# Performance work log

Hardware: AMD Instinct MI355X
Metric: run time of the kernel (lower is better)

Reference implementation:

```python
import jax, jax.numpy as jnp
import numpy as np
from jax import lax

T, B, V, N = 128, 256, 256, 1024


def setup_inputs() -> dict:
    key = jax.random.key(0)
    k1, k2, k3, k4 = jax.random.split(key, 4)
    inputs = jax.random.uniform(k1, (T, B, V), dtype=jnp.float32)
    labels = jax.random.uniform(k2, (T * B, V), dtype=jnp.float32)
    weights = jax.random.normal(k3, (V + N, N), dtype=jnp.float32) * 0.1
    bias = jnp.zeros((N,), dtype=jnp.float32)
    output_weights = jax.random.normal(k4, (N, V), dtype=jnp.float32) * 0.1
    output_bias = jnp.zeros((V,), dtype=jnp.float32)
    return {
        "inputs": inputs,
        "labels": labels,
        "weights": weights,
        "bias": bias,
        "output_weights": output_weights,
        "output_bias": output_bias,
    }


def reference(inputs, labels, weights, bias, output_weights, output_bias):
    t, b, v = inputs.shape
    n = weights.shape[1]
    # split concat-matmul into x@Wx + h@Wh (same math as concat([x,h]) @ W)
    w_x = weights[:v]   # [V, N]
    w_h = weights[v:]   # [N, N]

    def step(h, x):
        h_new = jnp.tanh(x @ w_x + h @ w_h + bias)
        return h_new, h_new

    h0 = jnp.zeros((b, n), dtype=inputs.dtype)
    _, outputs = lax.scan(step, h0, inputs)          # [T, B, N]
    outputs = outputs.reshape(t * b, n)              # concat over time
    logits = outputs @ output_weights + output_bias  # [T*B, V]
    # softmax_cross_entropy_with_logits (soft labels), then mean
    log_p = jax.nn.log_softmax(logits, axis=-1)
    loss = jnp.mean(-jnp.sum(labels * log_p, axis=-1))
    return loss
```

## Files before the change

### kernel.cpp

```cpp
#include <hip/hip_runtime.h>
#include <math.h>

typedef __bf16 bf16;
typedef __attribute__((ext_vector_type(4))) __bf16 bf16x4;
typedef __attribute__((ext_vector_type(8))) __bf16 bf16x8;
typedef __attribute__((ext_vector_type(4))) float f32x4;

#define T_STEPS 128
#define B_SZ    256
#define V_SZ    256
#define N_SZ    1024
#define NROWS   (T_STEPS * B_SZ)
#define RSTR    68
#define LSTR    17
#define NGRP    16
#define NCB     16

__device__ __forceinline__ float fast_tanh(float x) {
    float e = __expf(2.0f * x);
    return 1.0f - 2.0f / (e + 1.0f);
}

__device__ __forceinline__ bf16x8 cvt_bf16x8(float4 a, float4 b) {
    bf16x8 r;
    r[0] = (bf16)a.x; r[1] = (bf16)a.y; r[2] = (bf16)a.z; r[3] = (bf16)a.w;
    r[4] = (bf16)b.x; r[5] = (bf16)b.y; r[6] = (bf16)b.z; r[7] = (bf16)b.w;
    return r;
}

__global__ __launch_bounds__(256) void k_prep(
    const float* __restrict__ weights,
    const float* __restrict__ out_w,
    bf16* __restrict__ Wxt,
    bf16* __restrict__ Wht,
    bf16* __restrict__ Wot)
{
    __shared__ float tile[32][33];
    int id = blockIdx.x;
    const float* src; bf16* dst; int R, C, tr, tc;
    if (id < 256) {
        src = weights; dst = Wxt; R = V_SZ; C = N_SZ;
        tr = (id & 7) * 32; tc = (id >> 3) * 32;
    } else if (id < 1280) {
        id -= 256;
        src = weights + (size_t)V_SZ * N_SZ; dst = Wht; R = N_SZ; C = N_SZ;
        tr = (id & 31) * 32; tc = (id >> 5) * 32;
    } else {
        id -= 1280;
        src = out_w; dst = Wot; R = N_SZ; C = V_SZ;
        tr = (id & 31) * 32; tc = (id >> 5) * 32;
    }
    int tx = threadIdx.x & 31;
    int ty = threadIdx.x >> 5;
#pragma unroll
    for (int i = 0; i < 32; i += 8)
        tile[ty + i][tx] = src[(size_t)(tr + ty + i) * C + tc + tx];
    __syncthreads();
#pragma unroll
    for (int i = 0; i < 32; i += 8)
        dst[(size_t)(tc + ty + i) * R + tr + tx] = (bf16)tile[tx][ty + i];
}

__global__ __launch_bounds__(512, 2) void k_rnn(
    const float* __restrict__ Xf,
    const bf16* __restrict__ Wxt,
    const bf16* __restrict__ Wht,
    const bf16* __restrict__ Wot,
    const float* __restrict__ bias,
    bf16* __restrict__ XH,
    unsigned int* __restrict__ Lgu,
    int* __restrict__ flg)
{
    __shared__ float red[8 * 16 * RSTR];
    __shared__ float lred[8 * 16 * LSTR];
    const int tid  = threadIdx.x;
    const int lane = tid & 63;
    const int w    = tid >> 6;
    const int quad = lane >> 4;
    const int l15  = lane & 15;
    const int g  = blockIdx.x >> 4;
    const int c  = blockIdx.x & 15;
    const int m0 = g * 16;
    const int n0 = c * 64;
    const int k0 = w * 128;
    const int v0 = w * 32;
    int* gflg  = flg + g * (NCB * T_STEPS);
    int* myflg = gflg + c * T_STEPS;
    int* pflg  = gflg + (2 * w + (lane & 1)) * T_STEPS;

    const bf16* Bp = Wht + (size_t)(n0 + l15) * N_SZ + k0 + quad * 8;
    bf16x8 b[4][4];
#pragma unroll
    for (int nt = 0; nt < 4; ++nt)
#pragma unroll
        for (int kc = 0; kc < 4; ++kc)
            b[nt][kc] = *(const bf16x8*)&Bp[(size_t)(nt * 16) * N_SZ + kc * 32];
    bf16x8 bx[4];
#pragma unroll
    for (int nt = 0; nt < 4; ++nt)
        bx[nt] = *(const bf16x8*)&Wxt[(size_t)(n0 + nt * 16 + l15) * V_SZ + v0 + quad * 8];
    bf16x8 bo[4];
#pragma unroll
    for (int kc = 0; kc < 4; ++kc)
        bo[kc] = *(const bf16x8*)&Wot[(size_t)(c * 16 + l15) * N_SZ + k0 + kc * 32 + quad * 8];

    const int orow = tid >> 5;
    const int ocol = (tid & 31) * 2;
    const float bias0 = bias[n0 + ocol];
    const float bias1 = bias[n0 + ocol + 1];
    const int lrow = w * 2 + (lane >> 3);
    const int lvp  = lane & 7;
    unsigned int* XHu = (unsigned int*)XH;
    const f32x4 zz = {0.f, 0.f, 0.f, 0.f};
    const size_t xin = (size_t)(m0 + l15) * V_SZ + v0 + quad * 8;

    {
        float4 f0 = *(const float4*)&Xf[xin];
        float4 f1 = *(const float4*)&Xf[xin + 4];
        bf16x8 ax = cvt_bf16x8(f0, f1);
        f32x4 acc[4] = {zz, zz, zz, zz};
#pragma unroll
        for (int nt = 0; nt < 4; ++nt)
            acc[nt] = __builtin_amdgcn_mfma_f32_16x16x32_bf16(ax, bx[nt], acc[nt], 0, 0, 0);
#pragma unroll
        for (int nt = 0; nt < 4; ++nt)
#pragma unroll
            for (int r = 0; r < 4; ++r)
                red[(w * 16 + quad * 4 + r) * RSTR + nt * 16 + l15] = acc[nt][r];
        __syncthreads();
        float s0 = bias0, s1 = bias1;
#pragma unroll
        for (int w2 = 0; w2 < 8; ++w2) {
            float2 v = *(const float2*)&red[(w2 * 16 + orow) * RSTR + ocol];
            s0 += v.x; s1 += v.y;
        }
        bf16 r0 = (bf16)fast_tanh(s0);
        bf16 r1 = (bf16)fast_tanh(s1);
        unsigned int outw = (unsigned int)__builtin_bit_cast(unsigned short, r0)
                          | ((unsigned int)__builtin_bit_cast(unsigned short, r1) << 16);
        size_t oidx = (((size_t)m0 + orow) * N_SZ + n0 + ocol) >> 1;
        __hip_atomic_store(&XHu[oidx], outw, __ATOMIC_RELAXED, __HIP_MEMORY_SCOPE_AGENT);
        asm volatile("s_waitcnt vmcnt(0)" ::: "memory");
        __syncthreads();
        if (tid == 0)
            __hip_atomic_store(&myflg[0], 1, __ATOMIC_RELAXED, __HIP_MEMORY_SCOPE_AGENT);
    }

    for (int t = 1; t < T_STEPS; ++t) {
        float4 f0 = *(const float4*)&Xf[(size_t)t * B_SZ * V_SZ + xin];
        float4 f1 = *(const float4*)&Xf[(size_t)t * B_SZ * V_SZ + xin + 4];
        bf16x8 ax = cvt_bf16x8(f0, f1);
        f32x4 acc[4] = {zz, zz, zz, zz};
#pragma unroll
        for (int nt = 0; nt < 4; ++nt)
            acc[nt] = __builtin_amdgcn_mfma_f32_16x16x32_bf16(ax, bx[nt], acc[nt], 0, 0, 0);

        if (lane < 2) {
            while (__hip_atomic_load(&pflg[t - 1], __ATOMIC_RELAXED,
                                     __HIP_MEMORY_SCOPE_AGENT) == 0)
                __builtin_amdgcn_s_sleep(1);
        }
        asm volatile("" ::: "memory");

        const bf16* Ap = XH + ((size_t)(t - 1) * B_SZ + m0 + l15) * N_SZ + k0 + quad * 8;
        bf16x8 a[4];
#pragma unroll
        for (int kc = 0; kc < 4; ++kc)
            a[kc] = *(const bf16x8*)&Ap[kc * 32];

#pragma unroll
        for (int kc = 0; kc < 4; ++kc)
#pragma unroll
            for (int nt = 0; nt < 4; ++nt)
                acc[nt] = __builtin_amdgcn_mfma_f32_16x16x32_bf16(a[kc], b[nt][kc],
                                                                  acc[nt], 0, 0, 0);
#pragma unroll
        for (int nt = 0; nt < 4; ++nt)
#pragma unroll
            for (int r = 0; r < 4; ++r)
                red[(w * 16 + quad * 4 + r) * RSTR + nt * 16 + l15] = acc[nt][r];
        __syncthreads();

        float s0 = bias0, s1 = bias1;
#pragma unroll
        for (int w2 = 0; w2 < 8; ++w2) {
            float2 v = *(const float2*)&red[(w2 * 16 + orow) * RSTR + ocol];
            s0 += v.x; s1 += v.y;
        }
        bf16 r0 = (bf16)fast_tanh(s0);
        bf16 r1 = (bf16)fast_tanh(s1);
        unsigned int outw = (unsigned int)__builtin_bit_cast(unsigned short, r0)
                          | ((unsigned int)__builtin_bit_cast(unsigned short, r1) << 16);
        size_t oidx = (((size_t)t * B_SZ + m0 + orow) * N_SZ + n0 + ocol) >> 1;
        __hip_atomic_store(&XHu[oidx], outw, __ATOMIC_RELAXED, __HIP_MEMORY_SCOPE_AGENT);

        asm volatile("s_waitcnt vmcnt(0)" ::: "memory");
        __syncthreads();
        if (tid == 0)
            __hip_atomic_store(&myflg[t], 1, __ATOMIC_RELAXED, __HIP_MEMORY_SCOPE_AGENT);

        f32x4 lacc = zz;
#pragma unroll
        for (int kc = 0; kc < 4; ++kc)
            lacc = __builtin_amdgcn_mfma_f32_16x16x32_bf16(a[kc], bo[kc], lacc, 0, 0, 0);
#pragma unroll
        for (int r = 0; r < 4; ++r)
            lred[(w * 16 + quad * 4 + r) * LSTR + l15] = lacc[r];
        __syncthreads();
        if (lane < 16) {
            float sa = 0.f, sb = 0.f;
#pragma unroll
            for (int w2 = 0; w2 < 8; ++w2) {
                sa += lred[(w2 * 16 + lrow) * LSTR + lvp * 2];
                sb += lred[(w2 * 16 + lrow) * LSTR + lvp * 2 + 1];
            }
            bf16 pa = (bf16)sa, pb = (bf16)sb;
            unsigned int pw = (unsigned int)__builtin_bit_cast(unsigned short, pa)
                            | ((unsigned int)__builtin_bit_cast(unsigned short, pb) << 16);
            Lgu[(((size_t)(t - 1) * 16 + c) * B_SZ + m0 + lrow) * 8 + lvp] = pw;
        }
    }

    if (lane < 2) {
        while (__hip_atomic_load(&pflg[T_STEPS - 1], __ATOMIC_RELAXED,
                                 __HIP_MEMORY_SCOPE_AGENT) == 0)
            __builtin_amdgcn_s_sleep(1);
    }
    asm volatile("" ::: "memory");
    {
        const bf16* Ap = XH + ((size_t)(T_STEPS - 1) * B_SZ + m0 + l15) * N_SZ + k0 + quad * 8;
        bf16x8 a[4];
#pragma unroll
        for (int kc = 0; kc < 4; ++kc)
            a[kc] = *(const bf16x8*)&Ap[kc * 32];
        f32x4 lacc = zz;
#pragma unroll
        for (int kc = 0; kc < 4; ++kc)
            lacc = __builtin_amdgcn_mfma_f32_16x16x32_bf16(a[kc], bo[kc], lacc, 0, 0, 0);
        __syncthreads();
#pragma unroll
        for (int r = 0; r < 4; ++r)
            lred[(w * 16 + quad * 4 + r) * LSTR + l15] = lacc[r];
        __syncthreads();
        if (lane < 16) {
            float sa = 0.f, sb = 0.f;
#pragma unroll
            for (int w2 = 0; w2 < 8; ++w2) {
                sa += lred[(w2 * 16 + lrow) * LSTR + lvp * 2];
                sb += lred[(w2 * 16 + lrow) * LSTR + lvp * 2 + 1];
            }
            bf16 pa = (bf16)sa, pb = (bf16)sb;
            unsigned int pw = (unsigned int)__builtin_bit_cast(unsigned short, pa)
                            | ((unsigned int)__builtin_bit_cast(unsigned short, pb) << 16);
            Lgu[(((size_t)(T_STEPS - 1) * 16 + c) * B_SZ + m0 + lrow) * 8 + lvp] = pw;
        }
    }
}

__global__ __launch_bounds__(256) void k_lred(
    const bf16* __restrict__ Lg,
    const float* __restrict__ labels,
    const float* __restrict__ ob,
    float* __restrict__ out)
{
    __shared__ float bt[4];
    const int tid  = threadIdx.x;
    const int lane = tid & 63;
    const int w    = tid >> 6;
    const int cs   = lane >> 2;
    const int vi   = (lane & 3) * 4;
    const float4 ob4 = *(const float4*)&ob[cs * 16 + vi];

    float wtot = 0.f;
    for (int i = 0; i < 32; ++i) {
        int row  = blockIdx.x * 128 + w * 32 + i;
        int p    = row >> 8;
        int brow = row & 255;
        bf16x4 lv = *(const bf16x4*)&Lg[(((size_t)p * 16 + cs) * B_SZ + brow) * 16 + vi];
        float l0 = (float)lv.x + ob4.x;
        float l1 = (float)lv.y + ob4.y;
        float l2 = (float)lv.z + ob4.z;
        float l3 = (float)lv.w + ob4.w;
        float mx = fmaxf(fmaxf(l0, l1), fmaxf(l2, l3));
#pragma unroll
        for (int sft = 1; sft < 64; sft <<= 1)
            mx = fmaxf(mx, __shfl_xor(mx, sft, 64));
        float sume = __expf(l0 - mx) + __expf(l1 - mx) + __expf(l2 - mx) + __expf(l3 - mx);
        const float4 lb = *(const float4*)&labels[(size_t)row * V_SZ + cs * 16 + vi];
        float labs = lb.x + lb.y + lb.z + lb.w;
        float labv = lb.x * l0 + lb.y * l1 + lb.z * l2 + lb.w * l3;
#pragma unroll
        for (int sft = 1; sft < 64; sft <<= 1) {
            sume += __shfl_xor(sume, sft, 64);
            labs += __shfl_xor(labs, sft, 64);
            labv += __shfl_xor(labv, sft, 64);
        }
        float lse = mx + __logf(sume);
        wtot += labs * lse - labv;
    }
    if (lane == 0) bt[w] = wtot;
    __syncthreads();
    if (tid == 0)
        atomicAdd(out, (bt[0] + bt[1] + bt[2] + bt[3]) * (1.0f / (float)NROWS));
}

extern "C" void kernel_launch(void* const* d_in, const int* in_sizes, int n_in,
                              void* d_out, int out_size, void* d_ws, size_t ws_size,
                              hipStream_t stream)
{
    const float* inputs  = (const float*)d_in[0];
    const float* labels  = (const float*)d_in[1];
    const float* weights = (const float*)d_in[2];
    const float* bias    = (const float*)d_in[3];
    const float* out_w   = (const float*)d_in[4];
    const float* out_b   = (const float*)d_in[5];
    float* out = (float*)d_out;

    char* ws = (char*)d_ws;
    bf16* XH  = (bf16*)ws;  ws += (size_t)NROWS * N_SZ * 2;
    bf16* Lg  = (bf16*)ws;  ws += (size_t)NROWS * V_SZ * 2;
    bf16* Wxt = (bf16*)ws;  ws += (size_t)N_SZ * V_SZ * 2;
    bf16* Wht = (bf16*)ws;  ws += (size_t)N_SZ * N_SZ * 2;
    bf16* Wot = (bf16*)ws;  ws += (size_t)V_SZ * N_SZ * 2;
    int*  flg = (int*)ws;   ws += (size_t)NGRP * NCB * T_STEPS * 4;

    hipMemsetAsync(out, 0, sizeof(float), stream);
    hipMemsetAsync(flg, 0, (size_t)NGRP * NCB * T_STEPS * 4, stream);

    k_prep<<<dim3(1536), 256, 0, stream>>>(weights, out_w, Wxt, Wht, Wot);

    k_rnn<<<dim3(NGRP * NCB), 512, 0, stream>>>(inputs, Wxt, Wht, Wot, bias, XH,
                                                (unsigned int*)Lg, flg);

    k_lred<<<dim3(NROWS / 128), 256, 0, stream>>>(Lg, labels, out_b, out);
}
```

Before: 519.4 us.

## Give each RNN wave full-K ownership of one tile and move output projection into loss kernel

The recurrent kernel now assigns each wave a full 16x16 output tile over the whole K=1024 dimension with Wht held in registers. This removes the LDS cross-wave reduction and the __syncthreads calls per timestep, and flags become per-wave monotonic counters that all 64 lanes poll. The output projection and logits buffer are removed from the recurrence and recomputed in a separate tiled GEMM-plus-softmax loss kernel that reads XH. The trade-off is more register pressure (32+8 bf16x8 fragments), larger per-wave global loads of h each step, and more flag polling traffic.

New measurement: 1.138 ms. 2.19x slower.

```diff
diff --git a/kernel.cpp b/kernel.cpp
--- a/kernel.cpp
+++ b/kernel.cpp
@@ -2,7 +2,6 @@
 #include <math.h>
 
 typedef __bf16 bf16;
-typedef __attribute__((ext_vector_type(4))) __bf16 bf16x4;
 typedef __attribute__((ext_vector_type(8))) __bf16 bf16x8;
 typedef __attribute__((ext_vector_type(4))) float f32x4;
 
@@ -11,10 +10,8 @@
 #define V_SZ    256
 #define N_SZ    1024
 #define NROWS   (T_STEPS * B_SZ)
-#define RSTR    68
-#define LSTR    17
 #define NGRP    16
-#define NCB     16
+#define NTILE   64
 
 __device__ __forceinline__ float fast_tanh(float x) {
     float e = __expf(2.0f * x);
@@ -61,244 +58,206 @@
         dst[(size_t)(tc + ty + i) * R + tr + tx] = (bf16)tile[tx][ty + i];
 }
 
-__global__ __launch_bounds__(512, 2) void k_rnn(
+__global__ __launch_bounds__(256, 1) void k_rnn(
     const float* __restrict__ Xf,
     const bf16* __restrict__ Wxt,
     const bf16* __restrict__ Wht,
-    const bf16* __restrict__ Wot,
     const float* __restrict__ bias,
     bf16* __restrict__ XH,
-    unsigned int* __restrict__ Lgu,
     int* __restrict__ flg)
 {
-    __shared__ float red[8 * 16 * RSTR];
-    __shared__ float lred[8 * 16 * LSTR];
     const int tid  = threadIdx.x;
     const int lane = tid & 63;
     const int w    = tid >> 6;
     const int quad = lane >> 4;
     const int l15  = lane & 15;
-    const int g  = blockIdx.x >> 4;
-    const int c  = blockIdx.x & 15;
-    const int m0 = g * 16;
-    const int n0 = c * 64;
-    const int k0 = w * 128;
-    const int v0 = w * 32;
-    int* gflg  = flg + g * (NCB * T_STEPS);
-    int* myflg = gflg + c * T_STEPS;
-    int* pflg  = gflg + (2 * w + (lane & 1)) * T_STEPS;
-
-    const bf16* Bp = Wht + (size_t)(n0 + l15) * N_SZ + k0 + quad * 8;
-    bf16x8 b[4][4];
-#pragma unroll
-    for (int nt = 0; nt < 4; ++nt)
-#pragma unroll
-        for (int kc = 0; kc < 4; ++kc)
-            b[nt][kc] = *(const bf16x8*)&Bp[(size_t)(nt * 16) * N_SZ + kc * 32];
-    bf16x8 bx[4];
-#pragma unroll
-    for (int nt = 0; nt < 4; ++nt)
-        bx[nt] = *(const bf16x8*)&Wxt[(size_t)(n0 + nt * 16 + l15) * V_SZ + v0 + quad * 8];
-    bf16x8 bo[4];
-#pragma unroll
-    for (int kc = 0; kc < 4; ++kc)
-        bo[kc] = *(const bf16x8*)&Wot[(size_t)(c * 16 + l15) * N_SZ + k0 + kc * 32 + quad * 8];
-
-    const int orow = tid >> 5;
-    const int ocol = (tid & 31) * 2;
-    const float bias0 = bias[n0 + ocol];
-    const float bias1 = bias[n0 + ocol + 1];
-    const int lrow = w * 2 + (lane >> 3);
-    const int lvp  = lane & 7;
-    unsigned int* XHu = (unsigned int*)XH;
+    const int g    = blockIdx.x >> 4;
+    const int nt   = (blockIdx.x & 15) * 4 + w;
+    const int m0   = g * 16;
+    const int n0   = nt * 16;
+    int* gflg = flg + g * NTILE;
+
+    bf16x8 b[32];
+#pragma unroll
+    for (int kc = 0; kc < 32; ++kc)
+        b[kc] = *(const bf16x8*)&Wht[(size_t)(n0 + l15) * N_SZ + kc * 32 + quad * 8];
+    bf16x8 bx[8];
+#pragma unroll
+    for (int kc = 0; kc < 8; ++kc)
+        bx[kc] = *(const bf16x8*)&Wxt[(size_t)(n0 + l15) * V_SZ + kc * 32 + quad * 8];
+    const float4 bias4 = *(const float4*)&bias[n0 + quad * 4];
+
+    const size_t xbase = (size_t)(m0 + l15) * V_SZ + quad * 8;
+    const size_t hoff  = (size_t)(m0 + l15) * N_SZ + n0 + quad * 4;
     const f32x4 zz = {0.f, 0.f, 0.f, 0.f};
-    const size_t xin = (size_t)(m0 + l15) * V_SZ + v0 + quad * 8;
 
     {
-        float4 f0 = *(const float4*)&Xf[xin];
-        float4 f1 = *(const float4*)&Xf[xin + 4];
-        bf16x8 ax = cvt_bf16x8(f0, f1);
-        f32x4 acc[4] = {zz, zz, zz, zz};
-#pragma unroll
-        for (int nt = 0; nt < 4; ++nt)
-            acc[nt] = __builtin_amdgcn_mfma_f32_16x16x32_bf16(ax, bx[nt], acc[nt], 0, 0, 0);
-#pragma unroll
-        for (int nt = 0; nt < 4; ++nt)
-#pragma unroll
-            for (int r = 0; r < 4; ++r)
-                red[(w * 16 + quad * 4 + r) * RSTR + nt * 16 + l15] = acc[nt][r];
-        __syncthreads();
-        float s0 = bias0, s1 = bias1;
-#pragma unroll
-        for (int w2 = 0; w2 < 8; ++w2) {
-            float2 v = *(const float2*)&red[(w2 * 16 + orow) * RSTR + ocol];
-            s0 += v.x; s1 += v.y;
-        }
-        bf16 r0 = (bf16)fast_tanh(s0);
-        bf16 r1 = (bf16)fast_tanh(s1);
-        unsigned int outw = (unsigned int)__builtin_bit_cast(unsigned short, r0)
-                          | ((unsigned int)__builtin_bit_cast(unsigned short, r1) << 16);
-        size_t oidx = (((size_t)m0 + orow) * N_SZ + n0 + ocol) >> 1;
-        __hip_atomic_store(&XHu[oidx], outw, __ATOMIC_RELAXED, __HIP_MEMORY_SCOPE_AGENT);
+        f32x4 acc0 = zz, acc1 = zz;
+#pragma unroll
+        for (int kc = 0; kc < 8; ++kc) {
+            float4 f0 = *(const float4*)&Xf[xbase + kc * 32];
+            float4 f1 = *(const float4*)&Xf[xbase + kc * 32 + 4];
+            bf16x8 ax = cvt_bf16x8(f0, f1);
+            if (kc & 1) acc1 = __builtin_amdgcn_mfma_f32_16x16x32_bf16(bx[kc], ax, acc1, 0, 0, 0);
+            else        acc0 = __builtin_amdgcn_mfma_f32_16x16x32_bf16(bx[kc], ax, acc0, 0, 0, 0);
+        }
+        float s0 = acc0[0] + acc1[0] + bias4.x;
+        float s1 = acc0[1] + acc1[1] + bias4.y;
+        float s2 = acc0[2] + acc1[2] + bias4.z;
+        float s3 = acc0[3] + acc1[3] + bias4.w;
+        bf16 h0 = (bf16)fast_tanh(s0), h1 = (bf16)fast_tanh(s1);
+        bf16 h2 = (bf16)fast_tanh(s2), h3 = (bf16)fast_tanh(s3);
+        unsigned int lo = (unsigned int)__builtin_bit_cast(unsigned short, h0)
+                        | ((unsigned int)__builtin_bit_cast(unsigned short, h1) << 16);
+        unsigned int hi = (unsigned int)__builtin_bit_cast(unsigned short, h2)
+                        | ((unsigned int)__builtin_bit_cast(unsigned short, h3) << 16);
+        unsigned long long pk = (unsigned long long)lo | ((unsigned long long)hi << 32);
+        __hip_atomic_store((unsigned long long*)(XH + hoff), pk,
+                           __ATOMIC_RELAXED, __HIP_MEMORY_SCOPE_AGENT);
         asm volatile("s_waitcnt vmcnt(0)" ::: "memory");
-        __syncthreads();
-        if (tid == 0)
-            __hip_atomic_store(&myflg[0], 1, __ATOMIC_RELAXED, __HIP_MEMORY_SCOPE_AGENT);
+        if (lane == 0)
+            __hip_atomic_store(&gflg[nt], 1, __ATOMIC_RELAXED, __HIP_MEMORY_SCOPE_AGENT);
     }
 
     for (int t = 1; t < T_STEPS; ++t) {
-        float4 f0 = *(const float4*)&Xf[(size_t)t * B_SZ * V_SZ + xin];
-        float4 f1 = *(const float4*)&Xf[(size_t)t * B_SZ * V_SZ + xin + 4];
-        bf16x8 ax = cvt_bf16x8(f0, f1);
-        f32x4 acc[4] = {zz, zz, zz, zz};
-#pragma unroll
-        for (int nt = 0; nt < 4; ++nt)
-            acc[nt] = __builtin_amdgcn_mfma_f32_16x16x32_bf16(ax, bx[nt], acc[nt], 0, 0, 0);
-
-        if (lane < 2) {
-            while (__hip_atomic_load(&pflg[t - 1], __ATOMIC_RELAXED,
-                                     __HIP_MEMORY_SCOPE_AGENT) == 0)
-                __builtin_amdgcn_s_sleep(1);
+        f32x4 acc0 = zz, acc1 = zz;
+        const float* xp = &Xf[(size_t)t * B_SZ * V_SZ + xbase];
+#pragma unroll
+        for (int kc = 0; kc < 8; ++kc) {
+            float4 f0 = *(const float4*)&xp[kc * 32];
+            float4 f1 = *(const float4*)&xp[kc * 32 + 4];
+            bf16x8 ax = cvt_bf16x8(f0, f1);
+            if (kc & 1) acc1 = __builtin_amdgcn_mfma_f32_16x16x32_bf16(bx[kc], ax, acc1, 0, 0, 0);
+            else        acc0 = __builtin_amdgcn_mfma_f32_16x16x32_bf16(bx[kc], ax, acc0, 0, 0, 0);
+        }
+        asm volatile("" : "+v"(acc0), "+v"(acc1) :: "memory");
+
+        while (true) {
+            int v = __hip_atomic_load(&gflg[lane], __ATOMIC_RELAXED,
+                                      __HIP_MEMORY_SCOPE_AGENT);
+            if (__all(v >= t)) break;
+            __builtin_amdgcn_s_sleep(1);
         }
         asm volatile("" ::: "memory");
 
-        const bf16* Ap = XH + ((size_t)(t - 1) * B_SZ + m0 + l15) * N_SZ + k0 + quad * 8;
-        bf16x8 a[4];
-#pragma unroll
-        for (int kc = 0; kc < 4; ++kc)
+        const bf16* Ap = XH + ((size_t)(t - 1) * B_SZ + m0 + l15) * N_SZ + quad * 8;
+        bf16x8 a[32];
+#pragma unroll
+        for (int kc = 0; kc < 32; ++kc)
             a[kc] = *(const bf16x8*)&Ap[kc * 32];
-
-#pragma unroll
-        for (int kc = 0; kc < 4; ++kc)
-#pragma unroll
-            for (int nt = 0; nt < 4; ++nt)
-                acc[nt] = __builtin_amdgcn_mfma_f32_16x16x32_bf16(a[kc], b[nt][kc],
-                                                                  acc[nt], 0, 0, 0);
-#pragma unroll
-        for (int nt = 0; nt < 4; ++nt)
-#pragma unroll
-            for (int r = 0; r < 4; ++r)
-                red[(w * 16 + quad * 4 + r) * RSTR + nt * 16 + l15] = acc[nt][r];
-        __syncthreads();
-
-        float s0 = bias0, s1 = bias1;
-#pragma unroll
-        for (int w2 = 0; w2 < 8; ++w2) {
-            float2 v = *(const float2*)&red[(w2 * 16 + orow) * RSTR + ocol];
-            s0 += v.x; s1 += v.y;
-        }
-        bf16 r0 = (bf16)fast_tanh(s0);
-        bf16 r1 = (bf16)fast_tanh(s1);
-        unsigned int outw = (unsigned int)__builtin_bit_cast(unsigned short, r0)
-                          | ((unsigned int)__builtin_bit_cast(unsigned short, r1) << 16);
-        size_t oidx = (((size_t)t * B_SZ + m0 + orow) * N_SZ + n0 + ocol) >> 1;
-        __hip_atomic_store(&XHu[oidx], outw, __ATOMIC_RELAXED, __HIP_MEMORY_SCOPE_AGENT);
-
+#pragma unroll
+        for (int kc = 0; kc < 32; ++kc) {
+            if (kc & 1) acc1 = __builtin_amdgcn_mfma_f32_16x16x32_bf16(b[kc], a[kc], acc1, 0, 0, 0);
+            else        acc0 = __builtin_amdgcn_mfma_f32_16x16x32_bf16(b[kc], a[kc], acc0, 0, 0, 0);
+        }
+
+        float s0 = acc0[0] + acc1[0] + bias4.x;
+        float s1 = acc0[1] + acc1[1] + bias4.y;
+        float s2 = acc0[2] + acc1[2] + bias4.z;
+        float s3 = acc0[3] + acc1[3] + bias4.w;
+        bf16 h0 = (bf16)fast_tanh(s0), h1 = (bf16)fast_tanh(s1);
+        bf16 h2 = (bf16)fast_tanh(s2), h3 = (bf16)fast_tanh(s3);
+        unsigned int lo = (unsigned int)__builtin_bit_cast(unsigned short, h0)
+                        | ((unsigned int)__builtin_bit_cast(unsigned short, h1) << 16);
+        unsigned int hi = (unsigned int)__builtin_bit_cast(unsigned short, h2)
+                        | ((unsigned int)__builtin_bit_cast(unsigned short, h3) << 16);
+        unsigned long long pk = (unsigned long long)lo | ((unsigned long long)hi << 32);
+        __hip_atomic_store((unsigned long long*)(XH + (size_t)t * B_SZ * N_SZ + hoff), pk,
+                           __ATOMIC_RELAXED, __HIP_MEMORY_SCOPE_AGENT);
         asm volatile("s_waitcnt vmcnt(0)" ::: "memory");
-        __syncthreads();
-        if (tid == 0)
-            __hip_atomic_store(&myflg[t], 1, __ATOMIC_RELAXED, __HIP_MEMORY_SCOPE_AGENT);
-
-        f32x4 lacc = zz;
-#pragma unroll
-        for (int kc = 0; kc < 4; ++kc)
-            lacc = __builtin_amdgcn_mfma_f32_16x16x32_bf16(a[kc], bo[kc], lacc, 0, 0, 0);
-#pragma unroll
-        for (int r = 0; r < 4; ++r)
-            lred[(w * 16 + quad * 4 + r) * LSTR + l15] = lacc[r];
-        __syncthreads();
-        if (lane < 16) {
-            float sa = 0.f, sb = 0.f;
-#pragma unroll
-            for (int w2 = 0; w2 < 8; ++w2) {
-                sa += lred[(w2 * 16 + lrow) * LSTR + lvp * 2];
-                sb += lred[(w2 * 16 + lrow) * LSTR + lvp * 2 + 1];
-            }
-            bf16 pa = (bf16)sa, pb = (bf16)sb;
-            unsigned int pw = (unsigned int)__builtin_bit_cast(unsigned short, pa)
-                            | ((unsigned int)__builtin_bit_cast(unsigned short, pb) << 16);
-            Lgu[(((size_t)(t - 1) * 16 + c) * B_SZ + m0 + lrow) * 8 + lvp] = pw;
-        }
-    }
-
-    if (lane < 2) {
-        while (__hip_atomic_load(&pflg[T_STEPS - 1], __ATOMIC_RELAXED,
-                                 __HIP_MEMORY_SCOPE_AGENT) == 0)
-            __builtin_amdgcn_s_sleep(1);
-    }
-    asm volatile("" ::: "memory");
-    {
-        const bf16* Ap = XH + ((size_t)(T_STEPS - 1) * B_SZ + m0 + l15) * N_SZ + k0 + quad * 8;
-        bf16x8 a[4];
-#pragma unroll
-        for (int kc = 0; kc < 4; ++kc)
-            a[kc] = *(const bf16x8*)&Ap[kc * 32];
-        f32x4 lacc = zz;
-#pragma unroll
-        for (int kc = 0; kc < 4; ++kc)
-            lacc = __builtin_amdgcn_mfma_f32_16x16x32_bf16(a[kc], bo[kc], lacc, 0, 0, 0);
-        __syncthreads();
-#pragma unroll
-        for (int r = 0; r < 4; ++r)
-            lred[(w * 16 + quad * 4 + r) * LSTR + l15] = lacc[r];
-        __syncthreads();
-        if (lane < 16) {
-            float sa = 0.f, sb = 0.f;
-#pragma unroll
-            for (int w2 = 0; w2 < 8; ++w2) {
-                sa += lred[(w2 * 16 + lrow) * LSTR + lvp * 2];
-                sb += lred[(w2 * 16 + lrow) * LSTR + lvp * 2 + 1];
-            }
-            bf16 pa = (bf16)sa, pb = (bf16)sb;
-            unsigned int pw = (unsigned int)__builtin_bit_cast(unsigned short, pa)
-                            | ((unsigned int)__builtin_bit_cast(unsigned short, pb) << 16);
-            Lgu[(((size_t)(T_STEPS - 1) * 16 + c) * B_SZ + m0 + lrow) * 8 + lvp] = pw;
-        }
-    }
-}
-
-__global__ __launch_bounds__(256) void k_lred(
-    const bf16* __restrict__ Lg,
+        if (lane == 0)
+            __hip_atomic_store(&gflg[nt], t + 1, __ATOMIC_RELAXED, __HIP_MEMORY_SCOPE_AGENT);
+    }
+}
+
+__global__ __launch_bounds__(256, 2) void k_loss(
+    const bf16*  __restrict__ XH,
+    const bf16*  __restrict__ Wot,
     const float* __restrict__ labels,
     const float* __restrict__ ob,
     float* __restrict__ out)
 {
+    __shared__ float lg[64][260];
     __shared__ float bt[4];
     const int tid  = threadIdx.x;
     const int lane = tid & 63;
     const int w    = tid >> 6;
-    const int cs   = lane >> 2;
-    const int vi   = (lane & 3) * 4;
-    const float4 ob4 = *(const float4*)&ob[cs * 16 + vi];
-
-    float wtot = 0.f;
-    for (int i = 0; i < 32; ++i) {
-        int row  = blockIdx.x * 128 + w * 32 + i;
-        int p    = row >> 8;
-        int brow = row & 255;
-        bf16x4 lv = *(const bf16x4*)&Lg[(((size_t)p * 16 + cs) * B_SZ + brow) * 16 + vi];
-        float l0 = (float)lv.x + ob4.x;
-        float l1 = (float)lv.y + ob4.y;
-        float l2 = (float)lv.z + ob4.z;
-        float l3 = (float)lv.w + ob4.w;
-        float mx = fmaxf(fmaxf(l0, l1), fmaxf(l2, l3));
-#pragma unroll
-        for (int sft = 1; sft < 64; sft <<= 1)
-            mx = fmaxf(mx, __shfl_xor(mx, sft, 64));
-        float sume = __expf(l0 - mx) + __expf(l1 - mx) + __expf(l2 - mx) + __expf(l3 - mx);
-        const float4 lb = *(const float4*)&labels[(size_t)row * V_SZ + cs * 16 + vi];
-        float labs = lb.x + lb.y + lb.z + lb.w;
-        float labv = lb.x * l0 + lb.y * l1 + lb.z * l2 + lb.w * l3;
-#pragma unroll
-        for (int sft = 1; sft < 64; sft <<= 1) {
-            sume += __shfl_xor(sume, sft, 64);
-            labs += __shfl_xor(labs, sft, 64);
-            labv += __shfl_xor(labv, sft, 64);
-        }
-        float lse = mx + __logf(sume);
-        wtot += labs * lse - labv;
-    }
-    if (lane == 0) bt[w] = wtot;
+    const int quad = lane >> 4;
+    const int l15  = lane & 15;
+    const int r0   = blockIdx.x * 64;
+
+    const int prow = w * 16 + (lane >> 2);
+    const int q    = lane & 3;
+    float4 lb[16];
+#pragma unroll
+    for (int i = 0; i < 16; ++i)
+        lb[i] = *(const float4*)&labels[(size_t)(r0 + prow) * V_SZ + q * 64 + i * 4];
+
+    float obv[4];
+#pragma unroll
+    for (int ct = 0; ct < 4; ++ct)
+        obv[ct] = ob[(w * 4 + ct) * 16 + l15];
+
+    f32x4 acc[4][4];
+#pragma unroll
+    for (int rt = 0; rt < 4; ++rt)
+#pragma unroll
+        for (int ct = 0; ct < 4; ++ct)
+            acc[rt][ct] = (f32x4){0.f, 0.f, 0.f, 0.f};
+
+#pragma unroll 4
+    for (int kc = 0; kc < 32; ++kc) {
+        bf16x8 a[4], bo[4];
+#pragma unroll
+        for (int rt = 0; rt < 4; ++rt)
+            a[rt] = *(const bf16x8*)&XH[(size_t)(r0 + rt * 16 + l15) * N_SZ + kc * 32 + quad * 8];
+#pragma unroll
+        for (int ct = 0; ct < 4; ++ct)
+            bo[ct] = *(const bf16x8*)&Wot[(size_t)((w * 4 + ct) * 16 + l15) * N_SZ + kc * 32 + quad * 8];
+#pragma unroll
+        for (int rt = 0; rt < 4; ++rt)
+#pragma unroll
+            for (int ct = 0; ct < 4; ++ct)
+                acc[rt][ct] = __builtin_amdgcn_mfma_f32_16x16x32_bf16(a[rt], bo[ct],
+                                                                      acc[rt][ct], 0, 0, 0);
+    }
+#pragma unroll
+    for (int rt = 0; rt < 4; ++rt)
+#pragma unroll
+        for (int ct = 0; ct < 4; ++ct)
+#pragma unroll
+            for (int r = 0; r < 4; ++r)
+                lg[rt * 16 + quad * 4 + r][(w * 4 + ct) * 16 + l15] = acc[rt][ct][r] + obv[ct];
+    __syncthreads();
+
+    float mx = -1e30f;
+#pragma unroll
+    for (int i = 0; i < 16; ++i) {
+        float4 v = *(const float4*)&lg[prow][q * 64 + i * 4];
+        mx = fmaxf(mx, fmaxf(fmaxf(v.x, v.y), fmaxf(v.z, v.w)));
+    }
+    mx = fmaxf(mx, __shfl_xor(mx, 1, 64));
+    mx = fmaxf(mx, __shfl_xor(mx, 2, 64));
+    float se = 0.f, labs = 0.f, labv = 0.f;
+#pragma unroll
+    for (int i = 0; i < 16; ++i) {
+        float4 v = *(const float4*)&lg[prow][q * 64 + i * 4];
+        se += __expf(v.x - mx) + __expf(v.y - mx) + __expf(v.z - mx) + __expf(v.w - mx);
+        float4 l = lb[i];
+        labs += l.x + l.y + l.z + l.w;
+        labv += l.x * v.x + l.y * v.y + l.z * v.z + l.w * v.w;
+    }
+#pragma unroll
+    for (int s = 1; s < 4; s <<= 1) {
+        se   += __shfl_xor(se, s, 64);
+        labs += __shfl_xor(labs, s, 64);
+        labv += __shfl_xor(labv, s, 64);
+    }
+    float wt = (q == 0) ? (labs * (mx + __logf(se)) - labv) : 0.f;
+#pragma unroll
+    for (int s = 4; s < 64; s <<= 1)
+        wt += __shfl_xor(wt, s, 64);
+    if (lane == 0) bt[w] = wt;
     __syncthreads();
     if (tid == 0)
         atomicAdd(out, (bt[0] + bt[1] + bt[2] + bt[3]) * (1.0f / (float)NROWS));
@@ -318,19 +277,17 @@
 
     char* ws = (char*)d_ws;
     bf16* XH  = (bf16*)ws;  ws += (size_t)NROWS * N_SZ * 2;
-    bf16* Lg  = (bf16*)ws;  ws += (size_t)NROWS * V_SZ * 2;
     bf16* Wxt = (bf16*)ws;  ws += (size_t)N_SZ * V_SZ * 2;
     bf16* Wht = (bf16*)ws;  ws += (size_t)N_SZ * N_SZ * 2;
     bf16* Wot = (bf16*)ws;  ws += (size_t)V_SZ * N_SZ * 2;
-    int*  flg = (int*)ws;   ws += (size_t)NGRP * NCB * T_STEPS * 4;
+    int*  flg = (int*)ws;   ws += (size_t)NGRP * NTILE * 4;
 
     hipMemsetAsync(out, 0, sizeof(float), stream);
-    hipMemsetAsync(flg, 0, (size_t)NGRP * NCB * T_STEPS * 4, stream);
+    hipMemsetAsync(flg, 0, (size_t)NGRP * NTILE * 4, stream);
 
     k_prep<<<dim3(1536), 256, 0, stream>>>(weights, out_w, Wxt, Wht, Wot);
 
-    k_rnn<<<dim3(NGRP * NCB), 512, 0, stream>>>(inputs, Wxt, Wht, Wot, bias, XH,
-                                                (unsigned int*)Lg, flg);
-
-    k_lred<<<dim3(NROWS / 128), 256, 0, stream>>>(Lg, labels, out_b, out);
-}
+    k_rnn<<<dim3(256), 256, 0, stream>>>(inputs, Wxt, Wht, bias, XH, flg);
+
+    k_loss<<<dim3(NROWS / 64), 256, 0, stream>>>(XH, Wot, labels, out_b, out);
+}
```
